# Performance work log

Hardware: AMD Instinct MI355X
Metric: run time of the kernel (lower is better)

The kernel has to match this reference:

```python
import jax, jax.numpy as jnp
import numpy as np

D_MODEL = 1024
NUM_HEADS = 16
HEAD_DIM = D_MODEL // NUM_HEADS


def setup_inputs() -> dict:
    key = jax.random.key(0)
    ks = jax.random.split(key, 9)
    s = 1.0 / np.sqrt(D_MODEL)
    x = jax.random.normal(ks[0], (2, 2048, D_MODEL), dtype=jnp.float32)
    Wq = jax.random.uniform(ks[1], (D_MODEL, D_MODEL), jnp.float32, -s, s)
    bq = jax.random.uniform(ks[2], (D_MODEL,), jnp.float32, -s, s)
    Wk = jax.random.uniform(ks[3], (D_MODEL, D_MODEL), jnp.float32, -s, s)
    bk = jax.random.uniform(ks[4], (D_MODEL,), jnp.float32, -s, s)
    Wv = jax.random.uniform(ks[5], (D_MODEL, D_MODEL), jnp.float32, -s, s)
    bv = jax.random.uniform(ks[6], (D_MODEL,), jnp.float32, -s, s)
    Wo = jax.random.uniform(ks[7], (D_MODEL, D_MODEL), jnp.float32, -s, s)
    bo = jax.random.uniform(ks[8], (D_MODEL,), jnp.float32, -s, s)
    return {"x": x, "Wq": Wq, "bq": bq, "Wk": Wk, "bk": bk,
            "Wv": Wv, "bv": bv, "Wo": Wo, "bo": bo}


def reference(x, Wq, bq, Wk, bk, Wv, bv, Wo, bo):
    B, S, D = x.shape
    H, Hd = NUM_HEADS, HEAD_DIM
    # projections (torch Linear: x @ W.T + b; here W stored as [in, out])
    q = (x @ Wq + bq).reshape(B, S, H, Hd).transpose(0, 2, 1, 3)  # [B,H,S,Hd]
    k = (x @ Wk + bk).reshape(B, S, H, Hd).transpose(0, 2, 1, 3)
    v = (x @ Wv + bv).reshape(B, S, H, Hd).transpose(0, 2, 1, 3)
    scale = 1.0 / jnp.sqrt(jnp.asarray(Hd, dtype=x.dtype))
    scores = jnp.einsum('bhqd,bhkd->bhqk', q, k) * scale  # [B,H,S,S]
    attn = jax.nn.softmax(scores, axis=-1)
    out = jnp.einsum('bhqk,bhkd->bhqd', attn, v)  # [B,H,S,Hd]
    out = out.transpose(0, 2, 1, 3).reshape(B, S, D)
    return out @ Wo + bo
```

## Files before the change

kernel.cpp:

```cpp
#include <hip/hip_runtime.h>
#include <hip/hip_bf16.h>
#include <string.h>


#define DM 1024
#define S_LEN 2048
#define NH 16
#define HD 64

using u16 = unsigned short;
using u32 = unsigned int;

typedef short bf16x8 __attribute__((ext_vector_type(8)));
typedef float f32x4  __attribute__((ext_vector_type(4)));
typedef float f32x16 __attribute__((ext_vector_type(16)));
typedef unsigned int u32x2 __attribute__((ext_vector_type(2)));

__device__ __forceinline__ u16 f2bf(float f) {
    u32 i = __float_as_uint(f);
    u32 r = i + 0x7fffu + ((i >> 16) & 1u);
    return (u16)(r >> 16);
}
__device__ __forceinline__ u32 pk_bf16(float a, float b) {
    __hip_bfloat162 h = __float22bfloat162_rn(float2{a, b});
    u32 r; memcpy(&r, &h, 4);
    return r;
}

__global__ __launch_bounds__(256) void prep_x(const float* __restrict__ X, u16* __restrict__ out) {
    int i = (blockIdx.x * 256 + threadIdx.x) * 4;
    float4 v = *(const float4*)(X + i);
    *(uint2*)(out + i) = make_uint2(pk_bf16(v.x, v.y), pk_bf16(v.z, v.w));
}

__global__ __launch_bounds__(256) void prep_wt3(
    const float* __restrict__ W0, const float* __restrict__ W1, const float* __restrict__ W2,
    u16* __restrict__ T0, u16* __restrict__ T1, u16* __restrict__ T2)
{
    __shared__ u16 tile[64][72];
    const float* W = (blockIdx.z == 0) ? W0 : (blockIdx.z == 1) ? W1 : W2;
    u16* WT        = (blockIdx.z == 0) ? T0 : (blockIdx.z == 1) ? T1 : T2;
    const int t = threadIdx.x;
    const int n0 = blockIdx.x * 64, k0 = blockIdx.y * 64;
    #pragma unroll
    for (int it = 0; it < 4; it++) {
        int k = it * 16 + (t >> 4);
        int n = (t & 15) * 4;
        float4 v = *(const float4*)(W + (size_t)(k0 + k) * DM + n0 + n);
        tile[n + 0][k] = f2bf(v.x);
        tile[n + 1][k] = f2bf(v.y);
        tile[n + 2][k] = f2bf(v.z);
        tile[n + 3][k] = f2bf(v.w);
    }
    __syncthreads();
    int n = t >> 2, kg = (t & 3) * 16;
    uint4 a = *(const uint4*)&tile[n][kg];
    uint4 b = *(const uint4*)&tile[n][kg + 8];
    *(uint4*)(WT + (size_t)(n0 + n) * DM + k0 + kg)     = a;
    *(uint4*)(WT + (size_t)(n0 + n) * DM + k0 + kg + 8) = b;
}

__global__ __launch_bounds__(256) void prep_wt1(const float* __restrict__ W, u16* __restrict__ WT) {
    __shared__ u16 tile[64][72];
    const int t = threadIdx.x;
    const int n0 = blockIdx.x * 64, k0 = blockIdx.y * 64;
    #pragma unroll
    for (int it = 0; it < 4; it++) {
        int k = it * 16 + (t >> 4);
        int n = (t & 15) * 4;
        float4 v = *(const float4*)(W + (size_t)(k0 + k) * DM + n0 + n);
        tile[n + 0][k] = f2bf(v.x);
        tile[n + 1][k] = f2bf(v.y);
        tile[n + 2][k] = f2bf(v.z);
        tile[n + 3][k] = f2bf(v.w);
    }
    __syncthreads();
    int n = t >> 2, kg = (t & 3) * 16;
    uint4 a = *(const uint4*)&tile[n][kg];
    uint4 b = *(const uint4*)&tile[n][kg + 8];
    *(uint4*)(WT + (size_t)(n0 + n) * DM + k0 + kg)     = a;
    *(uint4*)(WT + (size_t)(n0 + n) * DM + k0 + kg + 8) = b;
}

__global__ __launch_bounds__(256, 3) void gemm_qkv_z(
    const u16* __restrict__ WQT, const u16* __restrict__ WKT, const u16* __restrict__ WVT,
    const u16* __restrict__ X,
    const float* __restrict__ bq, const float* __restrict__ bk, const float* __restrict__ bv,
    u16* __restrict__ outQ, u16* __restrict__ outK, u16* __restrict__ outVT)
{
    __shared__ u16 Ws[128][72];
    __shared__ u16 Xs[128][72];

    const int z = blockIdx.z;
    const u16* WT = (z == 0) ? WQT : (z == 1) ? WKT : WVT;

    const int t = threadIdx.x;
    const int w = t >> 6, lane = t & 63, quad = lane >> 4, l16 = lane & 15;
    const int Mb0 = blockIdx.x * 128;
    const int Nb0 = blockIdx.y * 128;
    const int mloc = (w & 1) * 64, nloc = (w >> 1) * 64;

    f32x4 acc[4][4];
    #pragma unroll
    for (int i = 0; i < 4; i++)
        #pragma unroll
        for (int j = 0; j < 4; j++) acc[i][j] = (f32x4){0.f, 0.f, 0.f, 0.f};

    const int sr = t >> 3, sc8 = (t & 7) * 8;

    for (int k0 = 0; k0 < DM; k0 += 64) {
        __syncthreads();
        #pragma unroll
        for (int i = 0; i < 4; i++) {
            int r = i * 32 + sr;
            *(uint4*)&Ws[r][sc8] = *(const uint4*)(WT + (size_t)(Mb0 + r) * DM + k0 + sc8);
            *(uint4*)&Xs[r][sc8] = *(const uint4*)(X  + (size_t)(Nb0 + r) * DM + k0 + sc8);
        }
        __syncthreads();

        #pragma unroll
        for (int ks = 0; ks < 2; ks++) {
            const int kk = ks * 32 + quad * 8;
            bf16x8 af[4], bf[4];
            #pragma unroll
            for (int mt = 0; mt < 4; mt++)
                af[mt] = *(const bf16x8*)&Ws[mloc + mt * 16 + l16][kk];
            #pragma unroll
            for (int nt = 0; nt < 4; nt++)
                bf[nt] = *(const bf16x8*)&Xs[nloc + nt * 16 + l16][kk];
            #pragma unroll
            for (int mt = 0; mt < 4; mt++)
                #pragma unroll
                for (int nt = 0; nt < 4; nt++)
                    acc[mt][nt] = __builtin_amdgcn_mfma_f32_16x16x32_bf16(af[mt], bf[nt], acc[mt][nt], 0, 0, 0);
        }
    }

    const float QS = 0.18033688f;
    if (z <= 1) {
        u16* outP = (z == 0) ? outQ : outK;
        const float* bias = (z == 0) ? bq : bk;
        const float scale = (z == 0) ? QS : 1.0f;
        #pragma unroll
        for (int mt = 0; mt < 4; mt++) {
            int nf0 = Mb0 + mloc + mt * 16 + quad * 4;
            int hh = nf0 >> 6, hd = nf0 & 63;
            float4 bb = *(const float4*)(bias + nf0);
            #pragma unroll
            for (int nt = 0; nt < 4; nt++) {
                int m = Nb0 + nloc + nt * 16 + l16;
                int b = m >> 11, s = m & 2047;
                size_t idx = (size_t)(b * NH + hh) * 131072 + (size_t)s * 64 + hd;
                *(uint2*)(outP + idx) = make_uint2(
                    pk_bf16((acc[mt][nt][0] + bb.x) * scale, (acc[mt][nt][1] + bb.y) * scale),
                    pk_bf16((acc[mt][nt][2] + bb.z) * scale, (acc[mt][nt][3] + bb.w) * scale));
            }
        }
    } else {
        #pragma unroll
        for (int mt = 0; mt < 4; mt++) {
            #pragma unroll
            for (int r = 0; r < 4; r++) {
                int nf = Mb0 + mloc + mt * 16 + quad * 4 + r;
                int hh = nf >> 6, hd = nf & 63;
                float bb = bv[nf];
                #pragma unroll
                for (int nt = 0; nt < 4; nt++) {
                    int m = Nb0 + nloc + nt * 16 + l16;
                    int b = m >> 11, s = m & 2047;
                    outVT[(size_t)(b * NH + hh) * 131072 + (size_t)hd * S_LEN + s]
                        = f2bf(acc[mt][nt][r] + bb);
                }
            }
        }
    }
}

__global__ __launch_bounds__(256) void gemm_out(
    const u16* __restrict__ A, const u16* __restrict__ B,
    const float* __restrict__ bias, float* __restrict__ of32)
{
    __shared__ u16 As[64][72];
    __shared__ u16 Bs[128][72];

    const int t = threadIdx.x;
    const int w = t >> 6, lane = t & 63, quad = lane >> 4, l16 = lane & 15;
    const int Mb0 = blockIdx.x * 64;
    const int Nb0 = blockIdx.y * 128;
    const int Mb = Mb0 + (w & 1) * 32;
    const int Nb = Nb0 + (w >> 1) * 64;
    const int mloc = (w & 1) * 32, nloc = (w >> 1) * 64;

    f32x4 acc[2][4];
    #pragma unroll
    for (int i = 0; i < 2; i++)
        #pragma unroll
        for (int j = 0; j < 4; j++) acc[i][j] = (f32x4){0.f, 0.f, 0.f, 0.f};

    const int sr = t >> 3, sc8 = (t & 7) * 8;

    for (int k0 = 0; k0 < DM; k0 += 64) {
        const int h = k0 >> 6;
        __syncthreads();
        #pragma unroll
        for (int i = 0; i < 2; i++) {
            int r = i * 32 + sr;
            *(uint4*)&As[r][sc8] = *(const uint4*)(A + (size_t)(Mb0 + r) * DM + k0 + sc8);
        }
        #pragma unroll
        for (int i = 0; i < 4; i++) {
            int r = i * 32 + sr;
            int m = Nb0 + r;
            int b = m >> 11, s = m & 2047;
            *(uint4*)&Bs[r][sc8] =
                *(const uint4*)(B + (size_t)(b * NH + h) * 131072 + (size_t)s * 64 + sc8);
        }
        __syncthreads();

        #pragma unroll
        for (int ks = 0; ks < 2; ks++) {
            const int kk = ks * 32 + quad * 8;
            bf16x8 a0 = *(const bf16x8*)&As[mloc + l16][kk];
            bf16x8 a1 = *(const bf16x8*)&As[mloc + 16 + l16][kk];
            #pragma unroll
            for (int nt = 0; nt < 4; nt++) {
                bf16x8 bf = *(const bf16x8*)&Bs[nloc + nt * 16 + l16][kk];
                acc[0][nt] = __builtin_amdgcn_mfma_f32_16x16x32_bf16(a0, bf, acc[0][nt], 0, 0, 0);
                acc[1][nt] = __builtin_amdgcn_mfma_f32_16x16x32_bf16(a1, bf, acc[1][nt], 0, 0, 0);
            }
        }
    }
    #pragma unroll
    for (int mt = 0; mt < 2; mt++) {
        int nf0 = Mb + mt * 16 + quad * 4;
        float4 bvv = *(const float4*)(bias + nf0);
        #pragma unroll
        for (int nt = 0; nt < 4; nt++) {
            int m = Nb + nt * 16 + l16;
            float4 o;
            o.x = acc[mt][nt][0] + bvv.x; o.y = acc[mt][nt][1] + bvv.y;
            o.z = acc[mt][nt][2] + bvv.z; o.w = acc[mt][nt][3] + bvv.w;
            *(float4*)(of32 + (size_t)m * DM + nf0) = o;
        }
    }
}

__global__ __launch_bounds__(256) void attn_mfma(
    const u16* __restrict__ Q, const u16* __restrict__ K, const u16* __restrict__ VT,
    u16* __restrict__ O)
{
    __shared__ u16 Ks[2][64][72];
    __shared__ u16 Vs[2][64][72];

    const int t = threadIdx.x;
    const int w = t >> 6, lane = t & 63;
    const int l32 = lane & 31, h = lane >> 5;
    const int bh = blockIdx.y;
    const int q0 = blockIdx.x * 128;
    const size_t base = (size_t)bh * 131072;

    const int qrow = q0 + w * 32 + l32;
    bf16x8 qf[4];
    #pragma unroll
    for (int ks = 0; ks < 4; ks++)
        qf[ks] = *(const bf16x8*)(Q + base + (size_t)qrow * 64 + ks * 16 + h * 8);

    const short onebf = (short)0x3F80;
    const bf16x8 ones = {onebf, onebf, onebf, onebf, onebf, onebf, onebf, onebf};

    f32x16 o[2], lacc;
    #pragma unroll
    for (int ht = 0; ht < 2; ht++)
        #pragma unroll
        for (int i = 0; i < 16; i++) o[ht][i] = 0.f;
    #pragma unroll
    for (int i = 0; i < 16; i++) lacc[i] = 0.f;

    const int sr = t >> 3;
    const int sc8 = (t & 7) * 8;
    const u16* Kg = K + base;
    const u16* Vg = VT + base;

    #pragma unroll
    for (int i = 0; i < 2; i++) {
        int r = i * 32 + sr;
        *(uint4*)&Ks[0][r][sc8] = *(const uint4*)(Kg + (size_t)r * 64 + sc8);
        *(uint4*)&Vs[0][r][sc8] = *(const uint4*)(Vg + (size_t)r * S_LEN + sc8);
    }
    __syncthreads();

    for (int kt = 0; kt < 32; kt++) {
        const int cur = kt & 1;
        uint4 kreg[2], vreg[2];
        if (kt < 31) {
            #pragma unroll
            for (int i = 0; i < 2; i++) {
                int r = i * 32 + sr;
                kreg[i] = *(const uint4*)(Kg + (size_t)((kt + 1) * 64 + r) * 64 + sc8);
                vreg[i] = *(const uint4*)(Vg + (size_t)r * S_LEN + (kt + 1) * 64 + sc8);
            }
        }

        #pragma unroll
        for (int kh = 0; kh < 2; kh++) {
            f32x16 s;
            #pragma unroll
            for (int i = 0; i < 16; i++) s[i] = 0.f;
            #pragma unroll
            for (int ks = 0; ks < 4; ks++) {
                bf16x8 kf = *(const bf16x8*)&Ks[cur][kh * 32 + l32][ks * 16 + h * 8];
                s = __builtin_amdgcn_mfma_f32_32x32x16_bf16(kf, qf[ks], s, 0, 0, 0);
            }
            float p[16];
            #pragma unroll
            for (int i = 0; i < 16; i++) p[i] = __builtin_amdgcn_exp2f(s[i]);
            u32 A0 = pk_bf16(p[0],  p[1]),  B0 = pk_bf16(p[2],  p[3]);
            u32 A1 = pk_bf16(p[4],  p[5]),  B1 = pk_bf16(p[6],  p[7]);
            u32 A2 = pk_bf16(p[8],  p[9]),  B2 = pk_bf16(p[10], p[11]);
            u32 A3 = pk_bf16(p[12], p[13]), B3 = pk_bf16(p[14], p[15]);
            u32x2 sA0 = __builtin_amdgcn_permlane32_swap(A0, A1, false, false);
            u32x2 sB0 = __builtin_amdgcn_permlane32_swap(B0, B1, false, false);
            u32x2 sA1 = __builtin_amdgcn_permlane32_swap(A2, A3, false, false);
            u32x2 sB1 = __builtin_amdgcn_permlane32_swap(B2, B3, false, false);
            union { bf16x8 v; u32 wd[4]; } fr0, fr1;
            fr0.wd[0] = sA0.x; fr0.wd[1] = sB0.x; fr0.wd[2] = sA0.y; fr0.wd[3] = sB0.y;
            fr1.wd[0] = sA1.x; fr1.wd[1] = sB1.x; fr1.wd[2] = sA1.y; fr1.wd[3] = sB1.y;

            lacc = __builtin_amdgcn_mfma_f32_32x32x16_bf16(fr0.v, ones, lacc, 0, 0, 0);
            lacc = __builtin_amdgcn_mfma_f32_32x32x16_bf16(fr1.v, ones, lacc, 0, 0, 0);

            #pragma unroll
            for (int ht = 0; ht < 2; ht++) {
                bf16x8 vf0 = *(const bf16x8*)&Vs[cur][ht * 32 + l32][kh * 32 + h * 8];
                o[ht] = __builtin_amdgcn_mfma_f32_32x32x16_bf16(fr0.v, vf0, o[ht], 0, 0, 0);
                bf16x8 vf1 = *(const bf16x8*)&Vs[cur][ht * 32 + l32][kh * 32 + 16 + h * 8];
                o[ht] = __builtin_amdgcn_mfma_f32_32x32x16_bf16(fr1.v, vf1, o[ht], 0, 0, 0);
            }
        }

        if (kt < 31) {
            #pragma unroll
            for (int i = 0; i < 2; i++) {
                int r = i * 32 + sr;
                *(uint4*)&Ks[cur ^ 1][r][sc8] = kreg[i];
                *(uint4*)&Vs[cur ^ 1][r][sc8] = vreg[i];
            }
        }
        __syncthreads();
    }

    float inv[16];
    #pragma unroll
    for (int r = 0; r < 16; r++) inv[r] = 1.0f / lacc[r];
    #pragma unroll
    for (int ht = 0; ht < 2; ht++)
        #pragma unroll
        for (int r = 0; r < 16; r++) {
            int q = q0 + w * 32 + (r & 3) + 8 * (r >> 2) + 4 * h;
            O[base + (size_t)q * 64 + ht * 32 + l32] = f2bf(o[ht][r] * inv[r]);
        }
}

extern "C" void kernel_launch(void* const* d_in, const int* in_sizes, int n_in,
                              void* d_out, int out_size, void* d_ws, size_t ws_size,
                              hipStream_t stream) {
    const float* x  = (const float*)d_in[0];
    const float* Wq = (const float*)d_in[1];
    const float* bq = (const float*)d_in[2];
    const float* Wk = (const float*)d_in[3];
    const float* bk = (const float*)d_in[4];
    const float* Wv = (const float*)d_in[5];
    const float* bv = (const float*)d_in[6];
    const float* Wo = (const float*)d_in[7];
    const float* bo = (const float*)d_in[8];
    float* out = (float*)d_out;

    u16* xbf = (u16*)d_out;
    u16* wqt = xbf + 4194304;
    u16* wkt = wqt + 1048576;
    u16* wvt = wkt + 1048576;

    u16* qws  = (u16*)d_ws;
    u16* kws  = qws + 4194304;
    u16* vtws = kws + 4194304;
    u16* wot  = kws;

    prep_x<<<4096, 256, 0, stream>>>(x, xbf);
    prep_wt3<<<dim3(16, 16, 3), 256, 0, stream>>>(Wq, Wk, Wv, wqt, wkt, wvt);

    gemm_qkv_z<<<dim3(8, 32, 3), 256, 0, stream>>>(wqt, wkt, wvt, xbf, bq, bk, bv,
                                                   qws, kws, vtws);

    attn_mfma<<<dim3(16, 32), 256, 0, stream>>>(qws, kws, vtws, qws);

    prep_wt1<<<dim3(16, 16), 256, 0, stream>>>(Wo, wot);
    gemm_out<<<dim3(16, 32), 256, 0, stream>>>(wot, qws, bo, out);
}
```

Measured before the change: 198.9 us.

## Split attention key range across two wave groups with shared-memory reduction

The attention kernel now launches 512 threads per block. Two groups of four waves each handle half of the key sequence for the same 128 queries, each with its own double-buffered K/V tiles. After the loop, the second group writes its partial output and row-sum accumulators to shared memory, and the first group adds them, normalizes and stores the result. This doubles the waves working on each query tile without changing the grid, aiming to hide latency better given only 512 blocks. The cost is more LDS, the final reduction and synchronization, and pressure from the launch-bounds register limit.

```diff
diff --git a/kernel.cpp b/kernel.cpp
--- a/kernel.cpp
+++ b/kernel.cpp
@@ -245,21 +245,21 @@
     }
 }
 
-__global__ __launch_bounds__(256) void attn_mfma(
+__global__ __launch_bounds__(512, 4) void attn_mfma(
     const u16* __restrict__ Q, const u16* __restrict__ K, const u16* __restrict__ VT,
     u16* __restrict__ O)
 {
-    __shared__ u16 Ks[2][64][72];
-    __shared__ u16 Vs[2][64][72];
+    __shared__ __align__(64) u16 smem[2][2][2][64][72];
 
     const int t = threadIdx.x;
     const int w = t >> 6, lane = t & 63;
+    const int wq = w & 3, half = w >> 2;
     const int l32 = lane & 31, h = lane >> 5;
     const int bh = blockIdx.y;
     const int q0 = blockIdx.x * 128;
     const size_t base = (size_t)bh * 131072;
 
-    const int qrow = q0 + w * 32 + l32;
+    const int qrow = q0 + wq * 32 + l32;
     bf16x8 qf[4];
     #pragma unroll
     for (int ks = 0; ks < 4; ks++)
@@ -281,25 +281,24 @@
     const u16* Kg = K + base;
     const u16* Vg = VT + base;
 
-    #pragma unroll
-    for (int i = 0; i < 2; i++) {
-        int r = i * 32 + sr;
-        *(uint4*)&Ks[0][r][sc8] = *(const uint4*)(Kg + (size_t)r * 64 + sc8);
-        *(uint4*)&Vs[0][r][sc8] = *(const uint4*)(Vg + (size_t)r * S_LEN + sc8);
-    }
+    *(uint4*)&smem[0][0][0][sr][sc8] = *(const uint4*)(Kg + (size_t)sr * 64 + sc8);
+    *(uint4*)&smem[0][1][0][sr][sc8] = *(const uint4*)(Kg + (size_t)(16 * 64 + sr) * 64 + sc8);
+    *(uint4*)&smem[1][0][0][sr][sc8] = *(const uint4*)(Vg + (size_t)sr * S_LEN + sc8);
+    *(uint4*)&smem[1][1][0][sr][sc8] = *(const uint4*)(Vg + (size_t)sr * S_LEN + 16 * 64 + sc8);
     __syncthreads();
 
-    for (int kt = 0; kt < 32; kt++) {
-        const int cur = kt & 1;
-        uint4 kreg[2], vreg[2];
-        if (kt < 31) {
-            #pragma unroll
-            for (int i = 0; i < 2; i++) {
-                int r = i * 32 + sr;
-                kreg[i] = *(const uint4*)(Kg + (size_t)((kt + 1) * 64 + r) * 64 + sc8);
-                vreg[i] = *(const uint4*)(Vg + (size_t)r * S_LEN + (kt + 1) * 64 + sc8);
-            }
-        }
+    for (int it = 0; it < 16; it++) {
+        const int cur = it & 1;
+        uint4 kra, krb, vra, vrb;
+        if (it < 15) {
+            kra = *(const uint4*)(Kg + (size_t)((it + 1) * 64 + sr) * 64 + sc8);
+            krb = *(const uint4*)(Kg + (size_t)((it + 17) * 64 + sr) * 64 + sc8);
+            vra = *(const uint4*)(Vg + (size_t)sr * S_LEN + (it + 1) * 64 + sc8);
+            vrb = *(const uint4*)(Vg + (size_t)sr * S_LEN + (it + 17) * 64 + sc8);
+        }
+
+        const u16 (*Ksc)[72] = smem[0][half][cur];
+        const u16 (*Vsc)[72] = smem[1][half][cur];
 
         #pragma unroll
         for (int kh = 0; kh < 2; kh++) {
@@ -308,7 +307,7 @@
             for (int i = 0; i < 16; i++) s[i] = 0.f;
             #pragma unroll
             for (int ks = 0; ks < 4; ks++) {
-                bf16x8 kf = *(const bf16x8*)&Ks[cur][kh * 32 + l32][ks * 16 + h * 8];
+                bf16x8 kf = *(const bf16x8*)&Ksc[kh * 32 + l32][ks * 16 + h * 8];
                 s = __builtin_amdgcn_mfma_f32_32x32x16_bf16(kf, qf[ks], s, 0, 0, 0);
             }
             float p[16];
@@ -331,34 +330,50 @@
 
             #pragma unroll
             for (int ht = 0; ht < 2; ht++) {
-                bf16x8 vf0 = *(const bf16x8*)&Vs[cur][ht * 32 + l32][kh * 32 + h * 8];
+                bf16x8 vf0 = *(const bf16x8*)&Vsc[ht * 32 + l32][kh * 32 + h * 8];
                 o[ht] = __builtin_amdgcn_mfma_f32_32x32x16_bf16(fr0.v, vf0, o[ht], 0, 0, 0);
-                bf16x8 vf1 = *(const bf16x8*)&Vs[cur][ht * 32 + l32][kh * 32 + 16 + h * 8];
+                bf16x8 vf1 = *(const bf16x8*)&Vsc[ht * 32 + l32][kh * 32 + 16 + h * 8];
                 o[ht] = __builtin_amdgcn_mfma_f32_32x32x16_bf16(fr1.v, vf1, o[ht], 0, 0, 0);
             }
         }
 
-        if (kt < 31) {
-            #pragma unroll
-            for (int i = 0; i < 2; i++) {
-                int r = i * 32 + sr;
-                *(uint4*)&Ks[cur ^ 1][r][sc8] = kreg[i];
-                *(uint4*)&Vs[cur ^ 1][r][sc8] = vreg[i];
-            }
+        if (it < 15) {
+            *(uint4*)&smem[0][0][cur ^ 1][sr][sc8] = kra;
+            *(uint4*)&smem[0][1][cur ^ 1][sr][sc8] = krb;
+            *(uint4*)&smem[1][0][cur ^ 1][sr][sc8] = vra;
+            *(uint4*)&smem[1][1][cur ^ 1][sr][sc8] = vrb;
         }
         __syncthreads();
     }
 
-    float inv[16];
-    #pragma unroll
-    for (int r = 0; r < 16; r++) inv[r] = 1.0f / lacc[r];
-    #pragma unroll
-    for (int ht = 0; ht < 2; ht++)
-        #pragma unroll
-        for (int r = 0; r < 16; r++) {
-            int q = q0 + w * 32 + (r & 3) + 8 * (r >> 2) + 4 * h;
-            O[base + (size_t)q * 64 + ht * 32 + l32] = f2bf(o[ht][r] * inv[r]);
-        }
+    float* red = (float*)&smem[0][0][0][0][0];
+    if (half) {
+        #pragma unroll
+        for (int i = 0; i < 16; i++) {
+            red[((0 + wq) * 16 + i) * 64 + lane] = o[0][i];
+            red[((4 + wq) * 16 + i) * 64 + lane] = o[1][i];
+            red[((8 + wq) * 16 + i) * 64 + lane] = lacc[i];
+        }
+    }
+    __syncthreads();
+    if (!half) {
+        #pragma unroll
+        for (int i = 0; i < 16; i++) {
+            o[0][i] += red[((0 + wq) * 16 + i) * 64 + lane];
+            o[1][i] += red[((4 + wq) * 16 + i) * 64 + lane];
+            lacc[i] += red[((8 + wq) * 16 + i) * 64 + lane];
+        }
+        float inv[16];
+        #pragma unroll
+        for (int r = 0; r < 16; r++) inv[r] = 1.0f / lacc[r];
+        #pragma unroll
+        for (int ht = 0; ht < 2; ht++)
+            #pragma unroll
+            for (int r = 0; r < 16; r++) {
+                int q = q0 + wq * 32 + (r & 3) + 8 * (r >> 2) + 4 * h;
+                O[base + (size_t)q * 64 + ht * 32 + l32] = f2bf(o[ht][r] * inv[r]);
+            }
+    }
 }
 
 extern "C" void kernel_launch(void* const* d_in, const int* in_sizes, int n_in,
@@ -391,7 +406,7 @@
     gemm_qkv_z<<<dim3(8, 32, 3), 256, 0, stream>>>(wqt, wkt, wvt, xbf, bq, bk, bv,
                                                    qws, kws, vtws);
 
-    attn_mfma<<<dim3(16, 32), 256, 0, stream>>>(qws, kws, vtws, qws);
+    attn_mfma<<<dim3(16, 32), 512, 0, stream>>>(qws, kws, vtws, qws);
 
     prep_wt1<<<dim3(16, 16), 256, 0, stream>>>(Wo, wot);
     gemm_out<<<dim3(16, 32), 256, 0, stream>>>(wot, qws, bo, out);
```

Measured after the change: 197.8 us. About the same (-0.6%).
